# Performance work log

Hardware: AMD Instinct MI355X
Metric: run time of the kernel (lower is better)

Reference implementation:

```python
import jax, jax.numpy as jnp
import numpy as np

B, N, K = 8, 2048, 20
CIN, COUT, DIM, PH, MULT, UP = 256, 128, 64, 64, 4, 2
EPS = 1e-5

def _lin(k, o, i):
    return jax.random.normal(k, (o, i), jnp.float32) * (1.0 / np.sqrt(i))

def setup_inputs() -> dict:
    key = jax.random.key(0)
    ks = jax.random.split(key, 32)
    H = DIM * MULT
    return {
        'pos': jax.random.normal(ks[0], (B, 3, N), jnp.float32),
        'key_feat': jax.random.normal(ks[1], (B, CIN, N), jnp.float32),
        'query_feat': jax.random.normal(ks[2], (B, CIN, N), jnp.float32),
        'upfeat': jax.random.normal(ks[3], (B, CIN, N), jnp.float32),
        'mv_w1': _lin(ks[4], CIN, 2 * CIN), 'mv_b1': jnp.zeros(CIN),
        'mv_w2': _lin(ks[5], CIN, CIN), 'mv_b2': jnp.zeros(CIN),
        'mv_ws': _lin(ks[6], CIN, 2 * CIN), 'mv_bs': jnp.zeros(CIN),
        'wk': _lin(ks[7], DIM, CIN), 'bk': jnp.zeros(DIM),
        'wq': _lin(ks[8], DIM, CIN), 'bq': jnp.zeros(DIM),
        'wv': _lin(ks[9], DIM, CIN), 'bv': jnp.zeros(DIM),
        'wu': _lin(ks[10], DIM, CIN), 'bu': jnp.zeros(DIM),
        'pm_w1': _lin(ks[11], PH, 3), 'pm_b1': jnp.zeros(PH),
        'pm_g': jnp.ones(PH) + 0.1 * jax.random.normal(ks[12], (PH,)),
        'pm_be': 0.1 * jax.random.normal(ks[13], (PH,)),
        'pm_m': 0.1 * jax.random.normal(ks[14], (PH,)),
        'pm_v': jax.random.uniform(ks[15], (PH,), minval=0.5, maxval=1.5),
        'pm_w2': _lin(ks[16], DIM, PH), 'pm_b2': jnp.zeros(DIM),
        'am_w1': _lin(ks[17], H, DIM), 'am_b1': jnp.zeros(H),
        'am_g': jnp.ones(H) + 0.1 * jax.random.normal(ks[18], (H,)),
        'am_be': 0.1 * jax.random.normal(ks[19], (H,)),
        'am_m': 0.1 * jax.random.normal(ks[20], (H,)),
        'am_v': jax.random.uniform(ks[21], (H,), minval=0.5, maxval=1.5),
        'am_wt': jax.random.normal(ks[22], (H, DIM, UP), jnp.float32) * (1.0 / np.sqrt(H)),
        'am_bt': jnp.zeros(DIM),
        'we': _lin(ks[23], COUT, DIM), 'be': jnp.zeros(COUT),
        'wr': _lin(ks[24], COUT, CIN), 'br': jnp.zeros(COUT),
    }

def _c1(x, w, b):  # 1x1 Conv1d: x (B,C,N)
    return jnp.einsum('oc,bcn->bon', w, x) + b[None, :, None]

def _c2(x, w, b):  # 1x1 Conv2d: x (B,C,N,K)
    return jnp.einsum('oc,bcnk->bonk', w, x) + b[None, :, None, None]

def _bn(x, g, be, m, v):  # eval-mode BatchNorm2d over channel dim
    sc = g / jnp.sqrt(v + EPS)
    return x * sc[None, :, None, None] + (be - m * sc)[None, :, None, None]

def _group(f, idx):  # f (B,C,N), idx (B,N,K) -> (B,C,N,K)
    return jax.vmap(lambda fb, ib: fb[:, ib])(f, idx)

def reference(pos, key_feat, query_feat, upfeat, mv_w1, mv_b1, mv_w2, mv_b2, mv_ws, mv_bs, wk, bk, wq, bq, wv, bv, wu, bu, pm_w1, pm_b1, pm_g, pm_be, pm_m, pm_v, pm_w2, pm_b2, am_w1, am_b1, am_g, am_be, am_m, am_v, am_wt, am_bt, we, be, wr, br):
    # mlp_v: MLP_Res(in=2*CIN, hidden=CIN, out=CIN)
    x = jnp.concatenate([key_feat, query_feat], axis=1)
    value = _c1(jax.nn.relu(_c1(x, mv_w1, mv_b1)), mv_w2, mv_b2) + _c1(x, mv_ws, mv_bs)
    identity = value
    k = _c1(key_feat, wk, bk)
    q = _c1(query_feat, wq, bq)
    v = _c1(value, wv, bv)
    # self-KNN on pos
    pt = jnp.swapaxes(pos, 1, 2)  # (B,N,3)
    sq = jnp.sum(pt * pt, -1)
    d2 = sq[:, :, None] + sq[:, None, :] - 2.0 * jnp.einsum('bnc,bmc->bnm', pt, pt)
    _, idx = jax.lax.top_k(-d2, K)  # (B,N,K)
    k_g = _group(k, idx)
    qk_rel = q[..., None] - k_g  # (B,DIM,N,K)
    pos_rel = pos[..., None] - _group(pos, idx)  # (B,3,N,K)
    pe = _c2(jax.nn.relu(_bn(_c2(pos_rel, pm_w1, pm_b1), pm_g, pm_be, pm_m, pm_v)), pm_w2, pm_b2)
    uf = _c1(upfeat, wu, bu)
    uf_rel = uf[..., None] - _group(uf, idx)
    # attn_mlp: conv2d -> BN -> ReLU -> ConvTranspose2d((UP,1),(UP,1))
    h = jax.nn.relu(_bn(_c2(qk_rel + pe + uf_rel, am_w1, am_b1), am_g, am_be, am_m, am_v))  # (B,H,N,K)
    attn = jnp.einsum('bcnk,cor->bonrk', h, am_wt)  # (B,DIM,N,UP,K)
    b_, o_, n_, r_, k_ = attn.shape
    attn = attn.reshape(b_, o_, n_ * r_, k_) + am_bt[None, :, None, None]  # (B,DIM,UP*N,K)
    attn = jax.nn.softmax(attn, axis=-1)  # scale_layer = Softmax(dim=-1)
    val = _group(v, idx) + pe + uf_rel  # (B,DIM,N,K)
    val = jnp.repeat(val, UP, axis=2)  # nearest Upsample (UP,1)
    agg = jnp.sum(attn * val, axis=-1)  # (B,DIM,UP*N)
    y = _c1(agg, we, be)
    iden = jnp.repeat(_c1(identity, wr, br), UP, axis=2)
    return y + iden
```

## Files before the change

### kernel.cpp

```cpp
#include <hip/hip_runtime.h>
#include <hip/hip_bf16.h>

constexpr int B_ = 8, N_ = 2048, K_ = 20;
constexpr float EPS_ = 1e-5f;

constexpr int OW1P = 0;
constexpr int OWSP = OW1P + 256 * 256;
constexpr int OW2P = OWSP + 256 * 256;
constexpr int OWVP = OW2P + 128 * 256;
constexpr int OWRP = OWVP + 128 * 64;
constexpr int OWQT = OWRP + 128 * 128;
constexpr int OWKT = OWQT + 256 * 64;
constexpr int OWUT = OWKT + 256 * 64;
constexpr int OWET = OWUT + 256 * 64;
constexpr int OWTF = OWET + 64 * 128;
constexpr int OAWF = OWTF + 16384;
constexpr int OPWF = OAWF + 8192;
constexpr int OPW1 = OPWF + 2048;
constexpr int OB1  = OPW1 + 192;
constexpr int OBS2 = OB1 + 256;
constexpr int OBQ  = OBS2 + 256;
constexpr int OBK  = OBQ + 64;
constexpr int OBV  = OBK + 64;
constexpr int OBU  = OBV + 64;
constexpr int OBR  = OBU + 64;
constexpr int OBE  = OBR + 128;
constexpr int OPB1 = OBE + 128;
constexpr int OPSC = OPB1 + 64;
constexpr int OPSH = OPSC + 64;
constexpr int OPB2 = OPSH + 64;
constexpr int OASC = OPB2 + 64;
constexpr int OASH = OASC + 256;
constexpr int OAB1 = OASH + 256;
constexpr int OABT = OAB1 + 256;

constexpr size_t OFFB_WF   = 0;
constexpr size_t OFFB_IDX  = (size_t)2 << 20;
constexpr size_t OFFB_Q    = (size_t)4 << 20;
constexpr size_t OFFB_K    = (size_t)8 << 20;
constexpr size_t OFFB_U    = (size_t)12 << 20;
constexpr size_t OFFB_V    = (size_t)16 << 20;
constexpr size_t OFFB_IDEN = (size_t)20 << 20;

struct InPtrs { const float* p[38]; };

typedef _Float16 half2_t __attribute__((ext_vector_type(2)));
typedef _Float16 f16x8_t __attribute__((ext_vector_type(8)));
typedef float    f32x4_t __attribute__((ext_vector_type(4)));

union U4H8 { uint4 u; f16x8_t h; };

__device__ __forceinline__ unsigned pkh2(float a, float b) {
  union { unsigned u; half2_t h; } x;
  x.h = half2_t{(_Float16)a, (_Float16)b};
  return x.u;
}
__device__ __forceinline__ f32x4_t mfma_16x16x32(f16x8_t a, f16x8_t b, f32x4_t c) {
  return __builtin_amdgcn_mfma_f32_16x16x32_f16(a, b, c, 0, 0, 0);
}

__global__ __launch_bounds__(256) void k_prep(InPtrs in, float* __restrict__ wf) {
  const int tid = blockIdx.x * 256 + threadIdx.x;
  const int nth = gridDim.x * 256;
  const float *mv_w1 = in.p[4], *mv_b1 = in.p[5], *mv_w2 = in.p[6], *mv_b2 = in.p[7],
              *mv_ws = in.p[8], *mv_bs = in.p[9], *wk = in.p[10], *bk = in.p[11],
              *wq = in.p[12], *bq = in.p[13], *wv = in.p[14], *bv = in.p[15],
              *wu = in.p[16], *bu = in.p[17], *pm_w1 = in.p[18], *pm_b1 = in.p[19],
              *pm_g = in.p[20], *pm_be = in.p[21], *pm_m = in.p[22], *pm_v = in.p[23],
              *pm_w2 = in.p[24], *pm_b2 = in.p[25], *am_w1 = in.p[26], *am_b1 = in.p[27],
              *am_g = in.p[28], *am_be = in.p[29], *am_m = in.p[30], *am_v = in.p[31],
              *am_wt = in.p[32], *am_bt = in.p[33], *we = in.p[34], *be = in.p[35],
              *wr = in.p[36], *br = in.p[37];

  {
    unsigned* w1f = (unsigned*)(wf + OW1P);
    for (int i = tid; i < 65536; i += nth) {
      int q = i & 3, l = (i >> 2) & 63, ks = (i >> 8) & 15, mt = i >> 12;
      int m = mt * 16 + (l & 15);
      int k = ks * 32 + ((l >> 4) << 3) + 2 * q;
      w1f[i] = pkh2(mv_w1[m * 512 + k], mv_w1[m * 512 + k + 1]);
    }
    unsigned* wsf = (unsigned*)(wf + OWSP);
    for (int i = tid; i < 65536; i += nth) {
      int q = i & 3, l = (i >> 2) & 63, ks = (i >> 8) & 15, mt = i >> 12;
      int m = mt * 16 + (l & 15);
      int k = ks * 32 + ((l >> 4) << 3) + 2 * q;
      wsf[i] = pkh2(mv_ws[m * 512 + k], mv_ws[m * 512 + k + 1]);
    }
    unsigned* w2f = (unsigned*)(wf + OW2P);
    for (int i = tid; i < 32768; i += nth) {
      int q = i & 3, l = (i >> 2) & 63, ks = (i >> 8) & 7, mt = i >> 11;
      int m = mt * 16 + (l & 15);
      int k = ks * 32 + ((l >> 4) << 3) + 2 * q;
      w2f[i] = pkh2(mv_w2[m * 256 + k], mv_w2[m * 256 + k + 1]);
    }
    unsigned* wvf = (unsigned*)(wf + OWVP);
    for (int i = tid; i < 8192; i += nth) {
      int q = i & 3, l = (i >> 2) & 63, ks = (i >> 8) & 7, mt = i >> 11;
      int m = mt * 16 + (l & 15);
      int k = ks * 32 + ((l >> 4) << 3) + 2 * q;
      wvf[i] = pkh2(wv[m * 256 + k], wv[m * 256 + k + 1]);
    }
    unsigned* wrf = (unsigned*)(wf + OWRP);
    for (int i = tid; i < 16384; i += nth) {
      int q = i & 3, l = (i >> 2) & 63, ks = (i >> 8) & 7, mt = i >> 11;
      int m = mt * 16 + (l & 15);
      int k = ks * 32 + ((l >> 4) << 3) + 2 * q;
      wrf[i] = pkh2(wr[m * 256 + k], wr[m * 256 + k + 1]);
    }
    unsigned* wqf = (unsigned*)(wf + OWQT);
    for (int i = tid; i < 8192; i += nth) {
      int q = i & 3, l = (i >> 2) & 63, ks = (i >> 8) & 7, mt = i >> 11;
      int m = mt * 16 + (l & 15);
      int k = ks * 32 + ((l >> 4) << 3) + 2 * q;
      wqf[i] = pkh2(wq[m * 256 + k], wq[m * 256 + k + 1]);
    }
    unsigned* wkf = (unsigned*)(wf + OWKT);
    for (int i = tid; i < 8192; i += nth) {
      int q = i & 3, l = (i >> 2) & 63, ks = (i >> 8) & 7, mt = i >> 11;
      int m = mt * 16 + (l & 15);
      int k = ks * 32 + ((l >> 4) << 3) + 2 * q;
      wkf[i] = pkh2(wk[m * 256 + k], wk[m * 256 + k + 1]);
    }
  }
  for (int i = tid; i < 256 * 64; i += nth) { int c = i >> 6, m = i & 63; wf[OWUT + i] = wu[m * 256 + c]; }
  for (int i = tid; i < 64 * 128; i += nth) wf[OWET + i] = we[i];

  {
    unsigned* wtf = (unsigned*)(wf + OWTF);
    for (int i = tid; i < 16384; i += nth) {
      int q = i & 3, l = (i >> 2) & 63, ks = (i >> 8) & 7, mt = i >> 11;
      int orr = mt * 16 + (l & 15);
      int c = ks * 32 + ((l >> 4) << 3) + 2 * q;
      wtf[i] = pkh2(am_wt[c * 128 + orr], am_wt[(c + 1) * 128 + orr]);
    }
  }
  {
    unsigned* awf = (unsigned*)(wf + OAWF);
    for (int i = tid; i < 8192; i += nth) {
      int q = i & 3, l = (i >> 2) & 63, ks = (i >> 8) & 1, mt = i >> 9;
      int c = mt * 16 + (l & 15);
      int o = ks * 32 + ((l >> 4) << 3) + 2 * q;
      awf[i] = pkh2(am_w1[c * 64 + o], am_w1[c * 64 + o + 1]);
    }
  }
  {
    unsigned* pwf = (unsigned*)(wf + OPWF);
    for (int i = tid; i < 2048; i += nth) {
      int q = i & 3, l = (i >> 2) & 63, ks = (i >> 8) & 1, mt = i >> 9;
      int o = mt * 16 + (l & 15);
      int ph = ks * 32 + ((l >> 4) << 3) + 2 * q;
      pwf[i] = pkh2(pm_w2[o * 64 + ph], pm_w2[o * 64 + ph + 1]);
    }
  }
  for (int i = tid; i < 192; i += nth) wf[OPW1 + i] = pm_w1[i];
  for (int i = tid; i < 256; i += nth) {
    wf[OB1 + i] = mv_b1[i];
    wf[OBS2 + i] = mv_bs[i] + mv_b2[i];
    float sc = am_g[i] / sqrtf(am_v[i] + EPS_);
    wf[OASC + i] = sc;
    wf[OASH + i] = am_be[i] - am_m[i] * sc;
    wf[OAB1 + i] = am_b1[i];
  }
  for (int i = tid; i < 64; i += nth) {
    wf[OBQ + i] = bq[i]; wf[OBK + i] = bk[i];
    wf[OBV + i] = bv[i]; wf[OBU + i] = bu[i];
    wf[OABT + i] = am_bt[i]; wf[OPB1 + i] = pm_b1[i]; wf[OPB2 + i] = pm_b2[i];
    float sc = pm_g[i] / sqrtf(pm_v[i] + EPS_);
    wf[OPSC + i] = sc;
    wf[OPSH + i] = pm_be[i] - pm_m[i] * sc;
  }
  for (int i = tid; i < 128; i += nth) { wf[OBR + i] = br[i]; wf[OBE + i] = be[i]; }
}

__global__ __launch_bounds__(256, 2) void k_mv(const float* __restrict__ wf,
                                               const float* __restrict__ keyf,
                                               const float* __restrict__ qryf,
                                               float* __restrict__ vout,
                                               float* __restrict__ idenout,
                                               float* __restrict__ qout,
                                               float* __restrict__ kout) {
  const int b = blockIdx.y;
  const int n0 = blockIdx.x * 32;
  const int tid = threadIdx.x, lane = tid & 63, wid = tid >> 6;
  __shared__ __align__(16) char smem[49152];
  char* xsb = smem;
  char* hbb = smem + 32768;
  char* vbb = smem;

  {
    const int col = tid & 31, kq = tid >> 5;
    const int swz = (col & 7) << 4;
#pragma unroll 4
    for (int it = 0; it < 32; ++it) {
      int k2 = it * 8 + kq;
      int c = 2 * k2;
      const float* s = (c < 256) ? keyf : qryf;
      size_t base = ((size_t)b * 256 + (c & 255)) * N_ + n0 + col;
      float x0 = s[base], x1 = s[base + N_];
      *(unsigned*)(xsb + ((col * 1024 + k2 * 4) ^ swz)) = pkh2(x0, x1);
    }
  }
  __syncthreads();

  f32x4_t acch[4][2], accs[4][2];
#pragma unroll
  for (int m = 0; m < 4; ++m)
#pragma unroll
    for (int nt = 0; nt < 2; ++nt) {
      acch[m][nt] = f32x4_t{0.f, 0.f, 0.f, 0.f};
      accs[m][nt] = f32x4_t{0.f, 0.f, 0.f, 0.f};
    }
  {
    const uint4* w1f = (const uint4*)((const unsigned*)(wf + OW1P));
    const uint4* wsf = (const uint4*)((const unsigned*)(wf + OWSP));
#pragma unroll 2
    for (int ks = 0; ks < 16; ++ks) {
      U4H8 bu[2];
#pragma unroll
      for (int nt = 0; nt < 2; ++nt) {
        int col = nt * 16 + (lane & 15);
        bu[nt].u = *(const uint4*)(xsb + ((col * 1024 + ks * 64 + ((lane >> 4) << 4)) ^ ((col & 7) << 4)));
      }
#pragma unroll
      for (int m = 0; m < 4; ++m) {
        U4H8 a1, as_;
        a1.u = w1f[((wid * 4 + m) * 16 + ks) * 64 + lane];
        as_.u = wsf[((wid * 4 + m) * 16 + ks) * 64 + lane];
#pragma unroll
        for (int nt = 0; nt < 2; ++nt) {
          acch[m][nt] = mfma_16x16x32(a1.h, bu[nt].h, acch[m][nt]);
          accs[m][nt] = mfma_16x16x32(as_.h, bu[nt].h, accs[m][nt]);
        }
      }
    }
  }
#pragma unroll
  for (int m = 0; m < 4; ++m) {
    int ch0 = (wid * 4 + m) * 16 + ((lane >> 4) << 2);
    float4 b1v = *(const float4*)(wf + OB1 + ch0);
#pragma unroll
    for (int nt = 0; nt < 2; ++nt) {
      int col = nt * 16 + (lane & 15);
      float h0 = fmaxf(acch[m][nt][0] + b1v.x, 0.f);
      float h1 = fmaxf(acch[m][nt][1] + b1v.y, 0.f);
      float h2 = fmaxf(acch[m][nt][2] + b1v.z, 0.f);
      float h3 = fmaxf(acch[m][nt][3] + b1v.w, 0.f);
      uint2 p;
      p.x = pkh2(h0, h1);
      p.y = pkh2(h2, h3);
      *(uint2*)(hbb + ((col * 512 + ch0 * 2) ^ ((col & 7) << 4))) = p;
    }
  }

  {
    f32x4_t accq[2], acck[2];
#pragma unroll
    for (int nt = 0; nt < 2; ++nt) {
      accq[nt] = f32x4_t{0.f, 0.f, 0.f, 0.f};
      acck[nt] = f32x4_t{0.f, 0.f, 0.f, 0.f};
    }
    const uint4* wqf = (const uint4*)((const unsigned*)(wf + OWQT));
    const uint4* wkf = (const uint4*)((const unsigned*)(wf + OWKT));
#pragma unroll 2
    for (int ks8 = 0; ks8 < 8; ++ks8) {
      U4H8 bk_[2], bq_[2];
#pragma unroll
      for (int nt = 0; nt < 2; ++nt) {
        int col = nt * 16 + (lane & 15);
        int swz = (col & 7) << 4;
        bk_[nt].u = *(const uint4*)(xsb + ((col * 1024 + ks8 * 64 + ((lane >> 4) << 4)) ^ swz));
        bq_[nt].u = *(const uint4*)(xsb + ((col * 1024 + (8 + ks8) * 64 + ((lane >> 4) << 4)) ^ swz));
      }
      U4H8 aq, ak;
      aq.u = wqf[(wid * 8 + ks8) * 64 + lane];
      ak.u = wkf[(wid * 8 + ks8) * 64 + lane];
#pragma unroll
      for (int nt = 0; nt < 2; ++nt) {
        acck[nt] = mfma_16x16x32(ak.h, bk_[nt].h, acck[nt]);
        accq[nt] = mfma_16x16x32(aq.h, bq_[nt].h, accq[nt]);
      }
    }
    int ch0 = wid * 16 + ((lane >> 4) << 2);
    float4 bqv = *(const float4*)(wf + OBQ + ch0);
    float4 bkv = *(const float4*)(wf + OBK + ch0);
#pragma unroll
    for (int nt = 0; nt < 2; ++nt) {
      int col = nt * 16 + (lane & 15);
      *(float4*)(qout + ((size_t)b * N_ + n0 + col) * 64 + ch0) =
          make_float4(accq[nt][0] + bqv.x, accq[nt][1] + bqv.y,
                      accq[nt][2] + bqv.z, accq[nt][3] + bqv.w);
      *(float4*)(kout + ((size_t)b * N_ + n0 + col) * 64 + ch0) =
          make_float4(acck[nt][0] + bkv.x, acck[nt][1] + bkv.y,
                      acck[nt][2] + bkv.z, acck[nt][3] + bkv.w);
    }
  }
  __syncthreads();

  {
    f32x4_t acc2[4][2];
#pragma unroll
    for (int m = 0; m < 4; ++m)
#pragma unroll
      for (int nt = 0; nt < 2; ++nt) acc2[m][nt] = f32x4_t{0.f, 0.f, 0.f, 0.f};
    const uint4* w2f = (const uint4*)((const unsigned*)(wf + OW2P));
#pragma unroll 2
    for (int ks = 0; ks < 8; ++ks) {
      U4H8 bu[2];
#pragma unroll
      for (int nt = 0; nt < 2; ++nt) {
        int col = nt * 16 + (lane & 15);
        bu[nt].u = *(const uint4*)(hbb + ((col * 512 + ks * 64 + ((lane >> 4) << 4)) ^ ((col & 7) << 4)));
      }
#pragma unroll
      for (int m = 0; m < 4; ++m) {
        U4H8 a2;
        a2.u = w2f[((wid * 4 + m) * 8 + ks) * 64 + lane];
#pragma unroll
        for (int nt = 0; nt < 2; ++nt)
          acc2[m][nt] = mfma_16x16x32(a2.h, bu[nt].h, acc2[m][nt]);
      }
    }
#pragma unroll
    for (int m = 0; m < 4; ++m) {
      int ch0 = (wid * 4 + m) * 16 + ((lane >> 4) << 2);
      float4 bsv = *(const float4*)(wf + OBS2 + ch0);
#pragma unroll
      for (int nt = 0; nt < 2; ++nt) {
        int col = nt * 16 + (lane & 15);
        float v0 = acc2[m][nt][0] + accs[m][nt][0] + bsv.x;
        float v1 = acc2[m][nt][1] + accs[m][nt][1] + bsv.y;
        float v2 = acc2[m][nt][2] + accs[m][nt][2] + bsv.z;
        float v3 = acc2[m][nt][3] + accs[m][nt][3] + bsv.w;
        uint2 p;
        p.x = pkh2(v0, v1);
        p.y = pkh2(v2, v3);
        *(uint2*)(vbb + ((col * 512 + ch0 * 2) ^ ((col & 7) << 4))) = p;
      }
    }
  }
  __syncthreads();

  {
    f32x4_t accv[2], accr[2][2];
#pragma unroll
    for (int nt = 0; nt < 2; ++nt) {
      accv[nt] = f32x4_t{0.f, 0.f, 0.f, 0.f};
      accr[0][nt] = f32x4_t{0.f, 0.f, 0.f, 0.f};
      accr[1][nt] = f32x4_t{0.f, 0.f, 0.f, 0.f};
    }
    const uint4* wvf = (const uint4*)((const unsigned*)(wf + OWVP));
    const uint4* wrf = (const uint4*)((const unsigned*)(wf + OWRP));
#pragma unroll 2
    for (int ks = 0; ks < 8; ++ks) {
      U4H8 bu[2];
#pragma unroll
      for (int nt = 0; nt < 2; ++nt) {
        int col = nt * 16 + (lane & 15);
        bu[nt].u = *(const uint4*)(vbb + ((col * 512 + ks * 64 + ((lane >> 4) << 4)) ^ ((col & 7) << 4)));
      }
      U4H8 av;
      av.u = wvf[(wid * 8 + ks) * 64 + lane];
#pragma unroll
      for (int nt = 0; nt < 2; ++nt)
        accv[nt] = mfma_16x16x32(av.h, bu[nt].h, accv[nt]);
#pragma unroll
      for (int m2 = 0; m2 < 2; ++m2) {
        U4H8 ar;
        ar.u = wrf[((wid * 2 + m2) * 8 + ks) * 64 + lane];
#pragma unroll
        for (int nt = 0; nt < 2; ++nt)
          accr[m2][nt] = mfma_16x16x32(ar.h, bu[nt].h, accr[m2][nt]);
      }
    }
    {
      int ch0 = wid * 16 + ((lane >> 4) << 2);
      float4 bvv = *(const float4*)(wf + OBV + ch0);
#pragma unroll
      for (int nt = 0; nt < 2; ++nt) {
        int col = nt * 16 + (lane & 15);
        *(float4*)(vout + ((size_t)b * N_ + n0 + col) * 64 + ch0) =
            make_float4(accv[nt][0] + bvv.x, accv[nt][1] + bvv.y,
                        accv[nt][2] + bvv.z, accv[nt][3] + bvv.w);
      }
    }
#pragma unroll
    for (int m2 = 0; m2 < 2; ++m2) {
      int ch0 = (wid * 2 + m2) * 16 + ((lane >> 4) << 2);
      float4 brv = *(const float4*)(wf + OBR + ch0);
#pragma unroll
      for (int nt = 0; nt < 2; ++nt) {
        int col = nt * 16 + (lane & 15);
        *(float4*)(idenout + ((size_t)b * N_ + n0 + col) * 128 + ch0) =
            make_float4(accr[m2][nt][0] + brv.x, accr[m2][nt][1] + brv.y,
                        accr[m2][nt][2] + brv.z, accr[m2][nt][3] + brv.w);
      }
    }
  }
}

__global__ __launch_bounds__(256) void k_gemm_u(const float* __restrict__ wf,
                                                const float* __restrict__ x,
                                                float* __restrict__ out) {
  const int b = blockIdx.y;
  const int n0 = blockIdx.x * 64;
  const float* Wt = wf + OWUT;
  const float* bias = wf + OBU;
  __shared__ float ws_[16][64];
  __shared__ float xs_[16][64];
  const int tid = threadIdx.x, tm = tid & 15, tn = tid >> 4;
  float acc[4][4] = {};
  for (int kt = 0; kt < 256; kt += 16) {
    for (int i = tid; i < 1024; i += 256) {
      int kk = i >> 6, col = i & 63;
      ws_[kk][col] = Wt[(size_t)(kt + kk) * 64 + col];
      xs_[kk][col] = x[((size_t)b * 256 + kt + kk) * N_ + n0 + col];
    }
    __syncthreads();
#pragma unroll
    for (int kk = 0; kk < 16; ++kk) {
      float4 x4 = *(const float4*)&xs_[kk][tn * 4];
      float4 w4 = *(const float4*)&ws_[kk][tm * 4];
      float wv[4] = {w4.x, w4.y, w4.z, w4.w};
      float xv[4] = {x4.x, x4.y, x4.z, x4.w};
#pragma unroll
      for (int i = 0; i < 4; ++i)
#pragma unroll
        for (int j = 0; j < 4; ++j) acc[i][j] += wv[i] * xv[j];
    }
    __syncthreads();
  }
#pragma unroll
  for (int j = 0; j < 4; ++j) {
    *(float4*)(out + ((size_t)b * N_ + n0 + tn * 4 + j) * 64 + tm * 4) =
        make_float4(acc[0][j] + bias[tm * 4], acc[1][j] + bias[tm * 4 + 1],
                    acc[2][j] + bias[tm * 4 + 2], acc[3][j] + bias[tm * 4 + 3]);
  }
}

__device__ __forceinline__ unsigned long long bitonic64_(unsigned long long v,
                                                         int lane) {
#pragma unroll
  for (int k = 2; k <= 64; k <<= 1) {
#pragma unroll
    for (int j = k >> 1; j > 0; j >>= 1) {
      unsigned long long o = (unsigned long long)__shfl_xor((long long)v, j);
      bool up = (lane & k) == 0;
      bool lower = (lane & j) == 0;
      bool keepmin = (lower == up);
      unsigned long long mn = o < v ? o : v;
      unsigned long long mx = o < v ? v : o;
      v = keepmin ? mn : mx;
    }
  }
  return v;
}

__global__ __launch_bounds__(256, 8) void k_knn(const float* __restrict__ pos,
                                                int* __restrict__ idxout) {
  const int b = blockIdx.x >> 11, n = blockIdx.x & 2047;
  __shared__ unsigned long long wkeys[4][20];
  __shared__ unsigned long long cand[4][64];
  const int tid = threadIdx.x;
  const int lane = tid & 63, wv = tid >> 6;
  const float* pb = pos + (size_t)b * 3 * N_;
  const double xq = pb[n], yq = pb[N_ + n], zq = pb[2 * N_ + n];
  const double sq = xq * xq + yq * yq + zq * zq;
  unsigned long long key[8];
#pragma unroll
  for (int s = 0; s < 8; ++s) {
    int i = tid + s * 256;
    double x = pb[i], y = pb[N_ + i], z = pb[2 * N_ + i];
    double psq = x * x + y * y + z * z;
    double dot = xq * x + yq * y + zq * z;
    double d2 = fmax((sq + psq) - 2.0 * dot, 0.0);
    key[s] = ((unsigned long long)__double_as_longlong(d2) & ~0x7FFull) |
             (unsigned long long)i;
  }
  unsigned long long m = key[0];
#pragma unroll
  for (int s = 1; s < 8; ++s) m = key[s] < m ? key[s] : m;

  unsigned long long v = bitonic64_(m, lane);
  unsigned long long T = (unsigned long long)__shfl((long long)v, 19);

  int c = 0;
#pragma unroll
  for (int s = 0; s < 8; ++s) c += (key[s] <= T) ? 1 : 0;
  int inc = c;
#pragma unroll
  for (int d = 1; d < 64; d <<= 1) {
    int t = __shfl_up(inc, d);
    if (lane >= d) inc += t;
  }
  const int C = __shfl(inc, 63);
  const int off = inc - c;

  if (C <= 64) {
    int o2 = off;
#pragma unroll
    for (int s = 0; s < 8; ++s) {
      if (key[s] <= T) { cand[wv][o2] = key[s]; ++o2; }
    }
    __builtin_amdgcn_wave_barrier();
    asm volatile("s_waitcnt lgkmcnt(0)" ::: "memory");
    unsigned long long cv = (lane < C) ? cand[wv][lane] : ~0ull;
    cv = bitonic64_(cv, lane);
    if (lane < K_) wkeys[wv][lane] = cv;
  } else {
    for (int r = 0; r < K_; ++r) {
      unsigned long long bk = key[0];
#pragma unroll
      for (int s = 1; s < 8; ++s) bk = key[s] < bk ? key[s] : bk;
      unsigned long long wk = bk;
#pragma unroll
      for (int mm = 32; mm; mm >>= 1) {
        unsigned long long ok = (unsigned long long)__shfl_xor((long long)wk, mm);
        if (ok < wk) wk = ok;
      }
      if (lane == 0) wkeys[wv][r] = wk;
      const int widx = (int)(wk & 0x7FF);
#pragma unroll
      for (int s = 0; s < 8; ++s)
        if (widx == tid + s * 256) key[s] = ~0ull;
    }
  }
  __syncthreads();

  if (tid < 128) {
    const int w = tid >> 5, p = tid & 31;
    if (p < 20) {
      const unsigned long long Kk = wkeys[w][p];
      int rank = p;
#pragma unroll
      for (int w2 = 0; w2 < 4; ++w2) {
        if (w2 == w) continue;
        int lo = 0, hi = 20;
        while (lo < hi) {
          int mid = (lo + hi) >> 1;
          if (wkeys[w2][mid] < Kk) lo = mid + 1; else hi = mid;
        }
        rank += lo;
      }
      if (rank < K_)
        idxout[((size_t)b * N_ + n) * K_ + rank] = (int)(Kk & 0x7FF);
    }
  }
}

__global__ __launch_bounds__(256, 4) void k_attn(
    const float* __restrict__ wf,
    const float* __restrict__ qb, const float* __restrict__ kb,
    const float* __restrict__ vb, const float* __restrict__ ub,
    const float* __restrict__ idenb, const int* __restrict__ idxb,
    const float* __restrict__ pos, float* __restrict__ out) {
  const int lb = ((int)blockIdx.x & 7) * 1024 + ((int)blockIdx.x >> 3);
  const int b = lb >> 10, n0 = (lb & 1023) * 2;
  const int tid = threadIdx.x;
  const int lane = tid & 63, wid = tid >> 6;

  __shared__ __align__(16) char smem[38528];
  char*  Sb   = smem;
  char*  hb   = smem + 6144;
  char*  t1b  = smem + 6144;
  char*  peb  = smem + 12288;
  float* lg   = (float*)(smem + 6144);
  char*  svb  = smem + 30720;
  float* aggs = (float*)(smem + 36864);
  int*   idxs = (int*)(smem + 37888);
  float* prx  = (float*)(smem + 38048);
  float* pry  = (float*)(smem + 38208);
  float* prz  = (float*)(smem + 38368);

  if (tid < 40) {
    int qi = tid >= 20;
    idxs[tid] = idxb[((size_t)b * N_ + n0 + qi) * K_ + (tid - qi * 20)] & 2047;
  }
  __syncthreads();

  float sreg[10], vreg[10];
  {
    const int qi = wid >> 1;
    size_t rowq = ((size_t)b * N_ + n0 + qi) * 64;
    float qvo = qb[rowq + lane];
    float ufo = ub[rowq + lane];
#pragma unroll
    for (int t = 0; t < 10; ++t) {
      int col = wid * 10 + t;
      int j = idxs[col];
      size_t rowj = ((size_t)b * N_ + j) * 64;
      float kvv = kb[rowj + lane], vvv = vb[rowj + lane], uvv = ub[rowj + lane];
      float ur = ufo - uvv;
      sreg[t] = (qvo - kvv) + ur;
      vreg[t] = vvv + ur;
    }
    if (tid < 40) {
      int j = idxs[tid];
      int qn = n0 + (tid >= 20);
      const float* pp = pos + (size_t)b * 3 * N_;
      prx[tid] = pp[qn] - pp[j];
      pry[tid] = pp[N_ + qn] - pp[N_ + j];
      prz[tid] = pp[2 * N_ + qn] - pp[2 * N_ + j];
    }
  }
  __syncthreads();

  {
    int ph = lane;
    float w0 = wf[OPW1 + ph * 3], w1 = wf[OPW1 + ph * 3 + 1], w2 = wf[OPW1 + ph * 3 + 2];
    float pb1 = wf[OPB1 + ph], sc = wf[OPSC + ph], sh = wf[OPSH + ph];
#pragma unroll
    for (int t = 0; t < 10; ++t) {
      int col = wid * 10 + t;
      float u = pb1 + w0 * prx[col] + w1 * pry[col] + w2 * prz[col];
      float tv = fmaxf(u * sc + sh, 0.f);
      *(_Float16*)(t1b + ((col * 128 + ph * 2) ^ ((col & 7) << 4))) = (_Float16)tv;
    }
  }
  __syncthreads();

  {
    f32x4_t pacc[3];
#pragma unroll
    for (int nt = 0; nt < 3; ++nt) pacc[nt] = f32x4_t{0.f, 0.f, 0.f, 0.f};
    const int mt = wid;
#pragma unroll
    for (int ks = 0; ks < 2; ++ks) {
      U4H8 a;
      a.u = ((const uint4*)((const unsigned*)(wf + OPWF)))[(mt * 2 + ks) * 64 + lane];
#pragma unroll
      for (int nt = 0; nt < 3; ++nt) {
        int kc = nt * 16 + (lane & 15);
        U4H8 bu;
        bu.u = *(const uint4*)(t1b + ((kc * 128 + (ks * 32 + ((lane >> 4) << 3)) * 2) ^ ((kc & 7) << 4)));
        pacc[nt] = mfma_16x16x32(a.h, bu.h, pacc[nt]);
      }
    }
    const int o0 = mt * 16 + ((lane >> 4) << 2);
    float4 pb2v = *(const float4*)(wf + OPB2 + o0);
#pragma unroll
    for (int nt = 0; nt < 3; ++nt) {
      int kc = nt * 16 + (lane & 15);
      float4 o;
      o.x = pacc[nt][0] + pb2v.x; o.y = pacc[nt][1] + pb2v.y;
      o.z = pacc[nt][2] + pb2v.z; o.w = pacc[nt][3] + pb2v.w;
      *(float4*)(peb + ((kc * 256 + o0 * 4) ^ ((kc & 7) << 4))) = o;
    }
  }
  __syncthreads();

  {
#pragma unroll
    for (int t = 0; t < 10; ++t) {
      int col = wid * 10 + t;
      float pe = *(const float*)(peb + ((col * 256 + lane * 4) ^ ((col & 7) << 4)));
      float sv = sreg[t] + pe;
      float vv = vreg[t] + pe;
      *(_Float16*)(svb + col * 128 + lane * 2) = (_Float16)vv;
      *(_Float16*)(Sb + ((col * 128 + lane * 2) ^ ((col & 7) << 4))) = (_Float16)sv;
    }
  }
  __syncthreads();

#pragma unroll
  for (int pass = 0; pass < 2; ++pass) {
    const int mt0 = wid * 4 + pass * 2;
    f32x4_t acc[2][3];
#pragma unroll
    for (int m = 0; m < 2; ++m)
#pragma unroll
      for (int nt = 0; nt < 3; ++nt) acc[m][nt] = f32x4_t{0.f, 0.f, 0.f, 0.f};
#pragma unroll
    for (int ks = 0; ks < 2; ++ks) {
      U4H8 bfr[3];
#pragma unroll
      for (int nt = 0; nt < 3; ++nt) {
        int kc = nt * 16 + (lane & 15);
        bfr[nt].u = *(const uint4*)(Sb + ((kc * 128 + (ks * 32 + ((lane >> 4) << 3)) * 2) ^ ((kc & 7) << 4)));
      }
#pragma unroll
      for (int m = 0; m < 2; ++m) {
        U4H8 a;
        a.u = ((const uint4*)((const unsigned*)(wf + OAWF)))[((mt0 + m) * 2 + ks) * 64 + lane];
#pragma unroll
        for (int nt = 0; nt < 3; ++nt)
          acc[m][nt] = mfma_16x16x32(a.h, bfr[nt].h, acc[m][nt]);
      }
    }
#pragma unroll
    for (int m = 0; m < 2; ++m) {
      const int c0 = (mt0 + m) * 16 + ((lane >> 4) << 2);
      float4 ab1 = *(const float4*)(wf + OAB1 + c0);
      float4 asc = *(const float4*)(wf + OASC + c0);
      float4 ash = *(const float4*)(wf + OASH + c0);
#pragma unroll
      for (int nt = 0; nt < 3; ++nt) {
        int kc = nt * 16 + (lane & 15);
        float h0 = fmaxf((acc[m][nt][0] + ab1.x) * asc.x + ash.x, 0.f);
        float h1 = fmaxf((acc[m][nt][1] + ab1.y) * asc.y + ash.y, 0.f);
        float h2 = fmaxf((acc[m][nt][2] + ab1.z) * asc.z + ash.z, 0.f);
        float h3 = fmaxf((acc[m][nt][3] + ab1.w) * asc.w + ash.w, 0.f);
        uint2 p;
        p.x = pkh2(h0, h1);
        p.y = pkh2(h2, h3);
        *(uint2*)(hb + ((kc * 512 + c0 * 2) ^ ((kc & 7) << 4))) = p;
      }
    }
  }
  __syncthreads();

  {
    f32x4_t acc5[2][3];
#pragma unroll
    for (int m = 0; m < 2; ++m)
#pragma unroll
      for (int nt = 0; nt < 3; ++nt) acc5[m][nt] = f32x4_t{0.f, 0.f, 0.f, 0.f};
#pragma unroll
    for (int ks = 0; ks < 8; ++ks) {
      U4H8 bfr[3];
#pragma unroll
      for (int nt = 0; nt < 3; ++nt) {
        int kc = nt * 16 + (lane & 15);
        bfr[nt].u = *(const uint4*)(hb + ((kc * 512 + (ks * 32 + ((lane >> 4) << 3)) * 2) ^ ((kc & 7) << 4)));
      }
#pragma unroll
      for (int m = 0; m < 2; ++m) {
        U4H8 a;
        a.u = ((const uint4*)((const unsigned*)(wf + OWTF)))[((wid * 2 + m) * 8 + ks) * 64 + lane];
#pragma unroll
        for (int nt = 0; nt < 3; ++nt)
          acc5[m][nt] = mfma_16x16x32(a.h, bfr[nt].h, acc5[m][nt]);
      }
    }
    __syncthreads();
#pragma unroll
    for (int m = 0; m < 2; ++m) {
      const int or0 = (wid * 2 + m) * 16 + ((lane >> 4) << 2);
#pragma unroll
      for (int nt = 0; nt < 3; ++nt) {
        int kc = nt * 16 + (lane & 15);
        if (kc < 40) {
#pragma unroll
          for (int r = 0; r < 4; ++r) lg[kc * 129 + or0 + r] = acc5[m][nt][r];
        }
      }
    }
  }
  __syncthreads();

  {
    const int qsel = tid >> 7, orr = tid & 127, o = orr >> 1;
    float l[20];
#pragma unroll
    for (int kk = 0; kk < 20; ++kk) l[kk] = lg[(qsel * 20 + kk) * 129 + orr];
    float bt = wf[OABT + o];
    float m = -3.4e38f;
#pragma unroll
    for (int kk = 0; kk < 20; ++kk) { l[kk] += bt; m = fmaxf(m, l[kk]); }
    float s = 0.f;
#pragma unroll
    for (int kk = 0; kk < 20; ++kk) { l[kk] = expf(l[kk] - m); s += l[kk]; }
    float inv = 1.f / s;
    float a = 0.f;
#pragma unroll
    for (int kk = 0; kk < 20; ++kk)
      a += l[kk] * (float)(*(const _Float16*)(svb + (qsel * 20 + kk) * 128 + o * 2));
    aggs[qsel * 128 + orr] = a * inv;
  }
  __syncthreads();

  {
    const int co = tid & 127, r = tid >> 7;
    float y0 = wf[OBE + co], y1 = y0;
    const float* w = wf + OWET + co * 64;
#pragma unroll 4
    for (int o4 = 0; o4 < 16; ++o4) {
      float4 w4 = *(const float4*)(w + o4 * 4);
      const float wv[4] = {w4.x, w4.y, w4.z, w4.w};
#pragma unroll
      for (int j = 0; j < 4; ++j) {
        int oi = o4 * 4 + j;
        y0 += wv[j] * aggs[oi * 2 + r];
        y1 += wv[j] * aggs[128 + oi * 2 + r];
      }
    }
    float id0 = idenb[((size_t)b * N_ + n0) * 128 + co];
    float id1 = idenb[((size_t)b * N_ + n0 + 1) * 128 + co];
    size_t obase = ((size_t)b * 128 + co) * (size_t)(2 * N_);
    out[obase + 2 * n0 + r] = y0 + id0;
    out[obase + 2 * n0 + 2 + r] = y1 + id1;
  }
}

extern "C" void kernel_launch(void* const* d_in, const int* in_sizes, int n_in,
                              void* d_out, int out_size, void* d_ws, size_t ws_size,
                              hipStream_t stream) {
  (void)in_sizes; (void)n_in; (void)out_size; (void)ws_size;
  InPtrs ip;
  for (int i = 0; i < 38; ++i) ip.p[i] = (const float*)d_in[i];
  char* ws = (char*)d_ws;
  float* wf    = (float*)(ws + OFFB_WF);
  int*   idxb  = (int*)(ws + OFFB_IDX);
  float* qb    = (float*)(ws + OFFB_Q);
  float* kb    = (float*)(ws + OFFB_K);
  float* ubuf  = (float*)(ws + OFFB_U);
  float* vbuf  = (float*)(ws + OFFB_V);
  float* idenb = (float*)(ws + OFFB_IDEN);

  k_prep<<<dim3(256), dim3(256), 0, stream>>>(ip, wf);
  k_mv<<<dim3(64, 8), dim3(256), 0, stream>>>(wf, ip.p[1], ip.p[2], vbuf, idenb, qb, kb);
  k_gemm_u<<<dim3(32, 8), dim3(256), 0, stream>>>(wf, ip.p[3], ubuf);
  k_knn<<<dim3(B_ * N_), dim3(256), 0, stream>>>(ip.p[0], idxb);
  k_attn<<<dim3(B_ * N_ / 2), dim3(256), 0, stream>>>(wf, qb, kb, vbuf, ubuf, idenb, idxb,
                                                      ip.p[0], (float*)d_out);
}
```

Measured before the change: 436.9 us.

## Shrink attention shared memory by chunking hidden layer and fusing PE add

Cuts the k_attn shared-memory footprint from about 38.5KB to 26.8KB and raises the launch-bounds occupancy hint from 4 to 6 blocks. The 256-wide hidden activation is now produced and consumed in two 128-channel chunks, with the transposed-conv MFMA accumulating across chunks, so only half of h is staged at once. The positional-encoding add is fused into the MFMA epilogue, which reads the fp16 S and V staging buffers directly instead of writing a separate fp32 PE buffer and keeping S and V in registers. The cost is an extra barrier per chunk, fp16 rounding of S and V before the PE add, and possible register spills under the tighter occupancy target.

```diff
diff --git a/kernel.cpp b/kernel.cpp
--- a/kernel.cpp
+++ b/kernel.cpp
@@ -548,7 +548,7 @@
   }
 }
 
-__global__ __launch_bounds__(256, 4) void k_attn(
+__global__ __launch_bounds__(256, 6) void k_attn(
     const float* __restrict__ wf,
     const float* __restrict__ qb, const float* __restrict__ kb,
     const float* __restrict__ vb, const float* __restrict__ ub,
@@ -559,18 +559,18 @@
   const int tid = threadIdx.x;
   const int lane = tid & 63, wid = tid >> 6;
 
-  __shared__ __align__(16) char smem[38528];
+  __shared__ __align__(16) char smem[26784];
   char*  Sb   = smem;
+  char*  t1b  = smem + 6144;
+  char*  sb0  = smem + 12288;
   char*  hb   = smem + 6144;
-  char*  t1b  = smem + 6144;
-  char*  peb  = smem + 12288;
-  float* lg   = (float*)(smem + 6144);
-  char*  svb  = smem + 30720;
-  float* aggs = (float*)(smem + 36864);
-  int*   idxs = (int*)(smem + 37888);
-  float* prx  = (float*)(smem + 38048);
-  float* pry  = (float*)(smem + 38208);
-  float* prz  = (float*)(smem + 38368);
+  int*   idxs = (int*)(smem + 18432);
+  float* prx  = (float*)(smem + 18592);
+  float* pry  = (float*)(smem + 18752);
+  float* prz  = (float*)(smem + 18912);
+  float* lg   = (float*)smem;
+  char*  svb  = smem + 20640;
+  float* aggs = (float*)(smem + 25760);
 
   if (tid < 40) {
     int qi = tid >= 20;
@@ -578,7 +578,6 @@
   }
   __syncthreads();
 
-  float sreg[10], vreg[10];
   {
     const int qi = wid >> 1;
     size_t rowq = ((size_t)b * N_ + n0 + qi) * 64;
@@ -591,8 +590,9 @@
       size_t rowj = ((size_t)b * N_ + j) * 64;
       float kvv = kb[rowj + lane], vvv = vb[rowj + lane], uvv = ub[rowj + lane];
       float ur = ufo - uvv;
-      sreg[t] = (qvo - kvv) + ur;
-      vreg[t] = vvv + ur;
+      int ro = (col * 128 + lane * 2) ^ ((col & 7) << 4);
+      *(_Float16*)(sb0 + ro) = (_Float16)((qvo - kvv) + ur);
+      *(_Float16*)(svb + ro) = (_Float16)(vvv + ur);
     }
     if (tid < 40) {
       int j = idxs[tid];
@@ -641,108 +641,107 @@
 #pragma unroll
     for (int nt = 0; nt < 3; ++nt) {
       int kc = nt * 16 + (lane & 15);
-      float4 o;
-      o.x = pacc[nt][0] + pb2v.x; o.y = pacc[nt][1] + pb2v.y;
-      o.z = pacc[nt][2] + pb2v.z; o.w = pacc[nt][3] + pb2v.w;
-      *(float4*)(peb + ((kc * 256 + o0 * 4) ^ ((kc & 7) << 4))) = o;
-    }
-  }
-  __syncthreads();
-
-  {
-#pragma unroll
-    for (int t = 0; t < 10; ++t) {
-      int col = wid * 10 + t;
-      float pe = *(const float*)(peb + ((col * 256 + lane * 4) ^ ((col & 7) << 4)));
-      float sv = sreg[t] + pe;
-      float vv = vreg[t] + pe;
-      *(_Float16*)(svb + col * 128 + lane * 2) = (_Float16)vv;
-      *(_Float16*)(Sb + ((col * 128 + lane * 2) ^ ((col & 7) << 4))) = (_Float16)sv;
-    }
-  }
-  __syncthreads();
-
-#pragma unroll
-  for (int pass = 0; pass < 2; ++pass) {
-    const int mt0 = wid * 4 + pass * 2;
-    f32x4_t acc[2][3];
-#pragma unroll
-    for (int m = 0; m < 2; ++m)
-#pragma unroll
-      for (int nt = 0; nt < 3; ++nt) acc[m][nt] = f32x4_t{0.f, 0.f, 0.f, 0.f};
-#pragma unroll
-    for (int ks = 0; ks < 2; ++ks) {
-      U4H8 bfr[3];
-#pragma unroll
-      for (int nt = 0; nt < 3; ++nt) {
-        int kc = nt * 16 + (lane & 15);
-        bfr[nt].u = *(const uint4*)(Sb + ((kc * 128 + (ks * 32 + ((lane >> 4) << 3)) * 2) ^ ((kc & 7) << 4)));
+      if (kc < 40) {
+        int ro = (kc * 128 + o0 * 2) ^ ((kc & 7) << 4);
+        float pe0 = pacc[nt][0] + pb2v.x, pe1 = pacc[nt][1] + pb2v.y;
+        float pe2 = pacc[nt][2] + pb2v.z, pe3 = pacc[nt][3] + pb2v.w;
+        const _Float16* sp = (const _Float16*)(sb0 + ro);
+        _Float16* vp = (_Float16*)(svb + ro);
+        uint2 ps, pv;
+        ps.x = pkh2((float)sp[0] + pe0, (float)sp[1] + pe1);
+        ps.y = pkh2((float)sp[2] + pe2, (float)sp[3] + pe3);
+        pv.x = pkh2((float)vp[0] + pe0, (float)vp[1] + pe1);
+        pv.y = pkh2((float)vp[2] + pe2, (float)vp[3] + pe3);
+        *(uint2*)(Sb + ro) = ps;
+        *(uint2*)vp = pv;
+      }
+    }
+  }
+  __syncthreads();
+
+  f32x4_t acc5[2][3];
+#pragma unroll
+  for (int m = 0; m < 2; ++m)
+#pragma unroll
+    for (int nt = 0; nt < 3; ++nt) acc5[m][nt] = f32x4_t{0.f, 0.f, 0.f, 0.f};
+#pragma unroll
+  for (int c = 0; c < 2; ++c) {
+    {
+      f32x4_t acc[2][3];
+#pragma unroll
+      for (int m = 0; m < 2; ++m)
+#pragma unroll
+        for (int nt = 0; nt < 3; ++nt) acc[m][nt] = f32x4_t{0.f, 0.f, 0.f, 0.f};
+#pragma unroll
+      for (int ks = 0; ks < 2; ++ks) {
+        U4H8 bfr[3];
+#pragma unroll
+        for (int nt = 0; nt < 3; ++nt) {
+          int kc = nt * 16 + (lane & 15);
+          bfr[nt].u = *(const uint4*)(Sb + ((kc * 128 + (ks * 32 + ((lane >> 4) << 3)) * 2) ^ ((kc & 7) << 4)));
+        }
+#pragma unroll
+        for (int m = 0; m < 2; ++m) {
+          U4H8 a;
+          a.u = ((const uint4*)((const unsigned*)(wf + OAWF)))[((c * 8 + wid * 2 + m) * 2 + ks) * 64 + lane];
+#pragma unroll
+          for (int nt = 0; nt < 3; ++nt)
+            acc[m][nt] = mfma_16x16x32(a.h, bfr[nt].h, acc[m][nt]);
+        }
       }
 #pragma unroll
       for (int m = 0; m < 2; ++m) {
-        U4H8 a;
-        a.u = ((const uint4*)((const unsigned*)(wf + OAWF)))[((mt0 + m) * 2 + ks) * 64 + lane];
-#pragma unroll
-        for (int nt = 0; nt < 3; ++nt)
-          acc[m][nt] = mfma_16x16x32(a.h, bfr[nt].h, acc[m][nt]);
-      }
-    }
-#pragma unroll
-    for (int m = 0; m < 2; ++m) {
-      const int c0 = (mt0 + m) * 16 + ((lane >> 4) << 2);
-      float4 ab1 = *(const float4*)(wf + OAB1 + c0);
-      float4 asc = *(const float4*)(wf + OASC + c0);
-      float4 ash = *(const float4*)(wf + OASH + c0);
-#pragma unroll
-      for (int nt = 0; nt < 3; ++nt) {
-        int kc = nt * 16 + (lane & 15);
-        float h0 = fmaxf((acc[m][nt][0] + ab1.x) * asc.x + ash.x, 0.f);
-        float h1 = fmaxf((acc[m][nt][1] + ab1.y) * asc.y + ash.y, 0.f);
-        float h2 = fmaxf((acc[m][nt][2] + ab1.z) * asc.z + ash.z, 0.f);
-        float h3 = fmaxf((acc[m][nt][3] + ab1.w) * asc.w + ash.w, 0.f);
-        uint2 p;
-        p.x = pkh2(h0, h1);
-        p.y = pkh2(h2, h3);
-        *(uint2*)(hb + ((kc * 512 + c0 * 2) ^ ((kc & 7) << 4))) = p;
-      }
-    }
-  }
-  __syncthreads();
-
-  {
-    f32x4_t acc5[2][3];
-#pragma unroll
-    for (int m = 0; m < 2; ++m)
-#pragma unroll
-      for (int nt = 0; nt < 3; ++nt) acc5[m][nt] = f32x4_t{0.f, 0.f, 0.f, 0.f};
-#pragma unroll
-    for (int ks = 0; ks < 8; ++ks) {
-      U4H8 bfr[3];
-#pragma unroll
-      for (int nt = 0; nt < 3; ++nt) {
-        int kc = nt * 16 + (lane & 15);
-        bfr[nt].u = *(const uint4*)(hb + ((kc * 512 + (ks * 32 + ((lane >> 4) << 3)) * 2) ^ ((kc & 7) << 4)));
-      }
-#pragma unroll
-      for (int m = 0; m < 2; ++m) {
-        U4H8 a;
-        a.u = ((const uint4*)((const unsigned*)(wf + OWTF)))[((wid * 2 + m) * 8 + ks) * 64 + lane];
-#pragma unroll
-        for (int nt = 0; nt < 3; ++nt)
-          acc5[m][nt] = mfma_16x16x32(a.h, bfr[nt].h, acc5[m][nt]);
+        const int cg = (c * 8 + wid * 2 + m) * 16 + ((lane >> 4) << 2);
+        const int cl = (wid * 2 + m) * 16 + ((lane >> 4) << 2);
+        float4 ab1 = *(const float4*)(wf + OAB1 + cg);
+        float4 asc = *(const float4*)(wf + OASC + cg);
+        float4 ash = *(const float4*)(wf + OASH + cg);
+#pragma unroll
+        for (int nt = 0; nt < 3; ++nt) {
+          int kc = nt * 16 + (lane & 15);
+          float h0 = fmaxf((acc[m][nt][0] + ab1.x) * asc.x + ash.x, 0.f);
+          float h1 = fmaxf((acc[m][nt][1] + ab1.y) * asc.y + ash.y, 0.f);
+          float h2 = fmaxf((acc[m][nt][2] + ab1.z) * asc.z + ash.z, 0.f);
+          float h3 = fmaxf((acc[m][nt][3] + ab1.w) * asc.w + ash.w, 0.f);
+          uint2 p;
+          p.x = pkh2(h0, h1);
+          p.y = pkh2(h2, h3);
+          *(uint2*)(hb + ((kc * 256 + cl * 2) ^ ((kc & 7) << 4))) = p;
+        }
       }
     }
     __syncthreads();
-#pragma unroll
-    for (int m = 0; m < 2; ++m) {
-      const int or0 = (wid * 2 + m) * 16 + ((lane >> 4) << 2);
-#pragma unroll
-      for (int nt = 0; nt < 3; ++nt) {
-        int kc = nt * 16 + (lane & 15);
-        if (kc < 40) {
-#pragma unroll
-          for (int r = 0; r < 4; ++r) lg[kc * 129 + or0 + r] = acc5[m][nt][r];
+    {
+#pragma unroll
+      for (int ksl = 0; ksl < 4; ++ksl) {
+        U4H8 bfr[3];
+#pragma unroll
+        for (int nt = 0; nt < 3; ++nt) {
+          int kc = nt * 16 + (lane & 15);
+          bfr[nt].u = *(const uint4*)(hb + ((kc * 256 + (ksl * 32 + ((lane >> 4) << 3)) * 2) ^ ((kc & 7) << 4)));
         }
+#pragma unroll
+        for (int m = 0; m < 2; ++m) {
+          U4H8 a;
+          a.u = ((const uint4*)((const unsigned*)(wf + OWTF)))[((wid * 2 + m) * 8 + (c * 4 + ksl)) * 64 + lane];
+#pragma unroll
+          for (int nt = 0; nt < 3; ++nt)
+            acc5[m][nt] = mfma_16x16x32(a.h, bfr[nt].h, acc5[m][nt]);
+        }
+      }
+    }
+    __syncthreads();
+  }
+
+#pragma unroll
+  for (int m = 0; m < 2; ++m) {
+    const int or0 = (wid * 2 + m) * 16 + ((lane >> 4) << 2);
+#pragma unroll
+    for (int nt = 0; nt < 3; ++nt) {
+      int kc = nt * 16 + (lane & 15);
+      if (kc < 40) {
+#pragma unroll
+        for (int r = 0; r < 4; ++r) lg[kc * 129 + or0 + r] = acc5[m][nt][r];
       }
     }
   }
@@ -763,8 +762,10 @@
     float inv = 1.f / s;
     float a = 0.f;
 #pragma unroll
-    for (int kk = 0; kk < 20; ++kk)
-      a += l[kk] * (float)(*(const _Float16*)(svb + (qsel * 20 + kk) * 128 + o * 2));
+    for (int kk = 0; kk < 20; ++kk) {
+      int row = qsel * 20 + kk;
+      a += l[kk] * (float)(*(const _Float16*)(svb + ((row * 128 + o * 2) ^ ((row & 7) << 4))));
+    }
     aggs[qsel * 128 + orr] = a * inv;
   }
   __syncthreads();
```

New measurement: 490.7 us. 1.12x slower.

## Fuse upfeat projection into k_mv using fp16 MFMA and drop k_gemm_u

Applied to the files above, without the earlier changes.

Removes the separate scalar-FP32 k_gemm_u kernel and computes the upfeat 1x1 projection inside k_mv alongside the q/k projections. It uses packed half-precision MFMA fragments prepared in k_prep. Upfeat tiles are staged into an extra 16KB of shared memory, which grows the k_mv LDS footprint to 64KB and may reduce occupancy. It also lowers the precision of the u projection from FP32 to fp16 inputs.

```diff
diff --git a/kernel.cpp b/kernel.cpp
--- a/kernel.cpp
+++ b/kernel.cpp
@@ -122,8 +122,14 @@
       int k = ks * 32 + ((l >> 4) << 3) + 2 * q;
       wkf[i] = pkh2(wk[m * 256 + k], wk[m * 256 + k + 1]);
     }
-  }
-  for (int i = tid; i < 256 * 64; i += nth) { int c = i >> 6, m = i & 63; wf[OWUT + i] = wu[m * 256 + c]; }
+    unsigned* wuf = (unsigned*)(wf + OWUT);
+    for (int i = tid; i < 8192; i += nth) {
+      int q = i & 3, l = (i >> 2) & 63, ks = (i >> 8) & 7, mt = i >> 11;
+      int m = mt * 16 + (l & 15);
+      int k = ks * 32 + ((l >> 4) << 3) + 2 * q;
+      wuf[i] = pkh2(wu[m * 256 + k], wu[m * 256 + k + 1]);
+    }
+  }
   for (int i = tid; i < 64 * 128; i += nth) wf[OWET + i] = we[i];
 
   {
@@ -176,16 +182,19 @@
 __global__ __launch_bounds__(256, 2) void k_mv(const float* __restrict__ wf,
                                                const float* __restrict__ keyf,
                                                const float* __restrict__ qryf,
+                                               const float* __restrict__ upf,
                                                float* __restrict__ vout,
                                                float* __restrict__ idenout,
                                                float* __restrict__ qout,
-                                               float* __restrict__ kout) {
+                                               float* __restrict__ kout,
+                                               float* __restrict__ uout) {
   const int b = blockIdx.y;
   const int n0 = blockIdx.x * 32;
   const int tid = threadIdx.x, lane = tid & 63, wid = tid >> 6;
-  __shared__ __align__(16) char smem[49152];
+  __shared__ __align__(16) char smem[65536];
   char* xsb = smem;
   char* hbb = smem + 32768;
+  char* uxs = smem + 49152;
   char* vbb = smem;
 
   {
@@ -200,6 +209,13 @@
       float x0 = s[base], x1 = s[base + N_];
       *(unsigned*)(xsb + ((col * 1024 + k2 * 4) ^ swz)) = pkh2(x0, x1);
     }
+#pragma unroll 4
+    for (int it = 0; it < 16; ++it) {
+      int k2 = it * 8 + kq;
+      size_t base = ((size_t)b * 256 + 2 * k2) * N_ + n0 + col;
+      float x0 = upf[base], x1 = upf[base + N_];
+      *(unsigned*)(uxs + ((col * 512 + k2 * 4) ^ swz)) = pkh2(x0, x1);
+    }
   }
   __syncthreads();
 
@@ -254,36 +270,42 @@
   }
 
   {
-    f32x4_t accq[2], acck[2];
+    f32x4_t accq[2], acck[2], accu[2];
 #pragma unroll
     for (int nt = 0; nt < 2; ++nt) {
       accq[nt] = f32x4_t{0.f, 0.f, 0.f, 0.f};
       acck[nt] = f32x4_t{0.f, 0.f, 0.f, 0.f};
+      accu[nt] = f32x4_t{0.f, 0.f, 0.f, 0.f};
     }
     const uint4* wqf = (const uint4*)((const unsigned*)(wf + OWQT));
     const uint4* wkf = (const uint4*)((const unsigned*)(wf + OWKT));
+    const uint4* wuf = (const uint4*)((const unsigned*)(wf + OWUT));
 #pragma unroll 2
     for (int ks8 = 0; ks8 < 8; ++ks8) {
-      U4H8 bk_[2], bq_[2];
+      U4H8 bk_[2], bq_[2], bu_[2];
 #pragma unroll
       for (int nt = 0; nt < 2; ++nt) {
         int col = nt * 16 + (lane & 15);
         int swz = (col & 7) << 4;
         bk_[nt].u = *(const uint4*)(xsb + ((col * 1024 + ks8 * 64 + ((lane >> 4) << 4)) ^ swz));
         bq_[nt].u = *(const uint4*)(xsb + ((col * 1024 + (8 + ks8) * 64 + ((lane >> 4) << 4)) ^ swz));
-      }
-      U4H8 aq, ak;
+        bu_[nt].u = *(const uint4*)(uxs + ((col * 512 + ks8 * 64 + ((lane >> 4) << 4)) ^ swz));
+      }
+      U4H8 aq, ak, au;
       aq.u = wqf[(wid * 8 + ks8) * 64 + lane];
       ak.u = wkf[(wid * 8 + ks8) * 64 + lane];
+      au.u = wuf[(wid * 8 + ks8) * 64 + lane];
 #pragma unroll
       for (int nt = 0; nt < 2; ++nt) {
         acck[nt] = mfma_16x16x32(ak.h, bk_[nt].h, acck[nt]);
         accq[nt] = mfma_16x16x32(aq.h, bq_[nt].h, accq[nt]);
+        accu[nt] = mfma_16x16x32(au.h, bu_[nt].h, accu[nt]);
       }
     }
     int ch0 = wid * 16 + ((lane >> 4) << 2);
     float4 bqv = *(const float4*)(wf + OBQ + ch0);
     float4 bkv = *(const float4*)(wf + OBK + ch0);
+    float4 buv = *(const float4*)(wf + OBU + ch0);
 #pragma unroll
     for (int nt = 0; nt < 2; ++nt) {
       int col = nt * 16 + (lane & 15);
@@ -293,6 +315,9 @@
       *(float4*)(kout + ((size_t)b * N_ + n0 + col) * 64 + ch0) =
           make_float4(acck[nt][0] + bkv.x, acck[nt][1] + bkv.y,
                       acck[nt][2] + bkv.z, acck[nt][3] + bkv.w);
+      *(float4*)(uout + ((size_t)b * N_ + n0 + col) * 64 + ch0) =
+          make_float4(accu[nt][0] + buv.x, accu[nt][1] + buv.y,
+                      accu[nt][2] + buv.z, accu[nt][3] + buv.w);
     }
   }
   __syncthreads();
@@ -396,45 +421,6 @@
                         accr[m2][nt][2] + brv.z, accr[m2][nt][3] + brv.w);
       }
     }
-  }
-}
-
-__global__ __launch_bounds__(256) void k_gemm_u(const float* __restrict__ wf,
-                                                const float* __restrict__ x,
-                                                float* __restrict__ out) {
-  const int b = blockIdx.y;
-  const int n0 = blockIdx.x * 64;
-  const float* Wt = wf + OWUT;
-  const float* bias = wf + OBU;
-  __shared__ float ws_[16][64];
-  __shared__ float xs_[16][64];
-  const int tid = threadIdx.x, tm = tid & 15, tn = tid >> 4;
-  float acc[4][4] = {};
-  for (int kt = 0; kt < 256; kt += 16) {
-    for (int i = tid; i < 1024; i += 256) {
-      int kk = i >> 6, col = i & 63;
-      ws_[kk][col] = Wt[(size_t)(kt + kk) * 64 + col];
-      xs_[kk][col] = x[((size_t)b * 256 + kt + kk) * N_ + n0 + col];
-    }
-    __syncthreads();
-#pragma unroll
-    for (int kk = 0; kk < 16; ++kk) {
-      float4 x4 = *(const float4*)&xs_[kk][tn * 4];
-      float4 w4 = *(const float4*)&ws_[kk][tm * 4];
-      float wv[4] = {w4.x, w4.y, w4.z, w4.w};
-      float xv[4] = {x4.x, x4.y, x4.z, x4.w};
-#pragma unroll
-      for (int i = 0; i < 4; ++i)
-#pragma unroll
-        for (int j = 0; j < 4; ++j) acc[i][j] += wv[i] * xv[j];
-    }
-    __syncthreads();
-  }
-#pragma unroll
-  for (int j = 0; j < 4; ++j) {
-    *(float4*)(out + ((size_t)b * N_ + n0 + tn * 4 + j) * 64 + tm * 4) =
-        make_float4(acc[0][j] + bias[tm * 4], acc[1][j] + bias[tm * 4 + 1],
-                    acc[2][j] + bias[tm * 4 + 2], acc[3][j] + bias[tm * 4 + 3]);
   }
 }
 
@@ -808,8 +794,8 @@
   float* idenb = (float*)(ws + OFFB_IDEN);
 
   k_prep<<<dim3(256), dim3(256), 0, stream>>>(ip, wf);
-  k_mv<<<dim3(64, 8), dim3(256), 0, stream>>>(wf, ip.p[1], ip.p[2], vbuf, idenb, qb, kb);
-  k_gemm_u<<<dim3(32, 8), dim3(256), 0, stream>>>(wf, ip.p[3], ubuf);
+  k_mv<<<dim3(64, 8), dim3(256), 0, stream>>>(wf, ip.p[1], ip.p[2], ip.p[3],
+                                              vbuf, idenb, qb, kb, ubuf);
   k_knn<<<dim3(B_ * N_), dim3(256), 0, stream>>>(ip.p[0], idxb);
   k_attn<<<dim3(B_ * N_ / 2), dim3(256), 0, stream>>>(wf, qb, kb, vbuf, ubuf, idenb, idxb,
                                                       ip.p[0], (float*)d_out);
```

After: 412.5 us. 1.06x faster.
